# Optimization experiments

Measured on AMD Instinct MI355X. Metric: run time of the kernel, lower is better.

## Reference

```python
import jax, jax.numpy as jnp
import numpy as np

B, QL, KL, D, H = 2, 512, 8192, 1024, 8
HD = D // H  # head dim = 128


def setup_inputs() -> dict:
    key = jax.random.key(0)
    ks = jax.random.split(key, 12)
    s = 0.02
    return {
        "inputs_q": jax.random.normal(ks[0], (B, QL, D), jnp.float32),
        "inputs_k": jax.random.normal(ks[1], (B, KL, D), jnp.float32),
        "inputs_v": jax.random.normal(ks[2], (B, KL, D), jnp.float32),
        "attention_mask": jax.random.randint(ks[3], (B, QL, KL), 0, 2).astype(bool),
        "Wq": jax.random.normal(ks[4], (D, D), jnp.float32) * s,
        "bq": jnp.zeros((D,), jnp.float32),
        "Wk": jax.random.normal(ks[5], (D, D), jnp.float32) * s,
        "bk": jnp.zeros((D,), jnp.float32),
        "Wv": jax.random.normal(ks[6], (D, D), jnp.float32) * s,
        "bv": jnp.zeros((D,), jnp.float32),
        "Wf": jax.random.normal(ks[7], (D, D), jnp.float32) * s,
        "bf": jnp.zeros((D,), jnp.float32),
    }


def reference(inputs_q, inputs_k, inputs_v, attention_mask, Wq, bq, Wk, bk, Wv, bv, Wf, bf):
    # Projections (torch Linear: x @ W.T + b)
    q = inputs_q @ Wq.T + bq  # [B, QL, D]
    k = inputs_k @ Wk.T + bk  # [B, KL, D]
    v = inputs_v @ Wv.T + bv  # [B, KL, D]

    q = q.reshape(B, QL, H, HD)
    k = k.reshape(B, KL, H, HD)
    v = v.reshape(B, KL, H, HD)

    # scores [B, H, QL, KL]
    scores = jnp.einsum("bqhd,bkhd->bhqk", q, k)
    scale = 1.0 / np.sqrt(HD).astype(np.float32)
    scores = scores * scale
    large_k = jnp.float32(1e30)
    scores = jnp.where(attention_mask[:, None, :, :], scores, -large_k)

    probs = jax.nn.softmax(scores, axis=-1)
    # note: original calls self.dropout(normalized) but discards the result -> no-op

    summed = jnp.einsum("bhqk,bkhd->bqhd", probs, v).reshape(B, QL, H * HD)

    # wipe rows whose mask is all zero
    wipe = jnp.all(~attention_mask, axis=2, keepdims=True)  # [B, QL, 1]
    summed = jnp.where(wipe, jnp.zeros_like(summed), summed)

    return summed @ Wf.T + bf
```

## Files before the change

### kernel.cpp

```cpp
#include <hip/hip_runtime.h>
#include <hip/hip_bf16.h>
#include <math.h>

typedef __attribute__((ext_vector_type(4))) float fx4;
typedef __attribute__((ext_vector_type(4))) short sx4;
typedef __attribute__((ext_vector_type(8))) short sx8;
typedef unsigned long long u64;

#define MFMA16(a, b, c) __builtin_amdgcn_mfma_f32_16x16x16bf16_1k(a, b, c, 0, 0, 0)
#define MFMA32(a, b, c) __builtin_amdgcn_mfma_f32_16x16x32_bf16(a, b, c, 0, 0, 0)

__device__ __forceinline__ unsigned short f2bf(float f) {
  unsigned int u = __float_as_uint(f);
  return (unsigned short)((u + 0x7fffu + ((u >> 16) & 1u)) >> 16);
}

__device__ __forceinline__ unsigned cvtpk(float lo, float hi) {
  unsigned r;
  asm("v_cvt_pk_bf16_f32 %0, %1, %2" : "=v"(r) : "v"(lo), "v"(hi));
  return r;
}

typedef const __attribute__((address_space(1))) char* gc1p;
typedef __attribute__((address_space(3))) char* lc3p;
__device__ __forceinline__ void glds16(const void* g, const void* lds_uniform) {
  gc1p gp = (gc1p)(unsigned long long)(uintptr_t)g;
  lc3p lp = (lc3p)(unsigned)__builtin_amdgcn_readfirstlane((int)(unsigned)(uintptr_t)lds_uniform);
  __builtin_amdgcn_global_load_lds(gp, lp, 16, 0, 0);
}

__global__ __launch_bounds__(256) void k_prep(
    const float* __restrict__ Wq, const float* __restrict__ Wk,
    const float* __restrict__ Wv, const float* __restrict__ Wf, short* cwq,
    short* cwk, short* cwv, short* cwf) {
  const int bx = blockIdx.x;
  const int t = threadIdx.x;
  const int seg = bx >> 6;
  const float* s = seg == 0 ? Wq : seg == 1 ? Wk : seg == 2 ? Wv : Wf;
  short* d = seg == 0 ? cwq : seg == 1 ? cwk : seg == 2 ? cwv : cwf;
  const size_t base = (size_t)(bx & 63) * 16384;
#pragma unroll
  for (int it = 0; it < 4; it++) {
    const size_t i = base + (size_t)it * 4096 + (size_t)t * 16;
    const fx4 a0 = *(const fx4*)(s + i);
    const fx4 a1 = *(const fx4*)(s + i + 4);
    const fx4 a2 = *(const fx4*)(s + i + 8);
    const fx4 a3 = *(const fx4*)(s + i + 12);
    sx8 o0, o1;
    o0[0] = (short)f2bf(a0[0]); o0[1] = (short)f2bf(a0[1]);
    o0[2] = (short)f2bf(a0[2]); o0[3] = (short)f2bf(a0[3]);
    o0[4] = (short)f2bf(a1[0]); o0[5] = (short)f2bf(a1[1]);
    o0[6] = (short)f2bf(a1[2]); o0[7] = (short)f2bf(a1[3]);
    o1[0] = (short)f2bf(a2[0]); o1[1] = (short)f2bf(a2[1]);
    o1[2] = (short)f2bf(a2[2]); o1[3] = (short)f2bf(a2[3]);
    o1[4] = (short)f2bf(a3[0]); o1[5] = (short)f2bf(a3[1]);
    o1[6] = (short)f2bf(a3[2]); o1[7] = (short)f2bf(a3[3]);
    *(sx8*)(d + i) = o0;
    *(sx8*)(d + i + 8) = o1;
  }
}

template <int MODE, int MT>
__device__ __forceinline__ void gemm_pipe(short* sA, short* sB,
                                          const float* __restrict__ Af,
                                          const short* __restrict__ Bw,
                                          const float* __restrict__ bias,
                                          void* __restrict__ Cptr, int M, int N,
                                          float alpha, int bx) {
  constexpr int K = 1024;
  constexpr int NT = 16;
  const int tid = threadIdx.x;
  const int lane = tid & 63;
  const int w = tid >> 6;
  const int quad = lane >> 4;
  const int l16 = lane & 15;
  const int x7 = l16 & 7;
  int m0, n0;
  if (M >= 8192) {
    const int ml = bx & 7, nn = (bx >> 3) & 7, mh = bx >> 6;
    m0 = (mh * 8 + ml) * MT;
    n0 = nn << 7;
  } else {
    const int ntile = N >> 7;
    n0 = (bx % ntile) << 7;
    m0 = (bx / ntile) * MT;
  }
  constexpr int NI = (MT == 128) ? 4 : 2;
  constexpr int NJ = (MT == 128) ? 4 : 2;
  const int wm = (MT == 128) ? ((w >> 1) << 6) : 0;
  const int wn = (MT == 128) ? ((w & 1) << 6) : (w << 5);
  const fx4 fzero = {0.f, 0.f, 0.f, 0.f};
  fx4 acc[4][NI];
#pragma unroll
  for (int i = 0; i < 4; i++)
#pragma unroll
    for (int j = 0; j < NI; j++) acc[i][j] = fzero;

  const int srow = lane >> 3;
  const int scb = lane & 7;
  fx4 ra[2][NJ][2];

  auto ISSUE_B = [&](int t) {
#pragma unroll
    for (int j = 0; j < 4; j++) {
      const int row = w * 32 + j * 8 + srow;
      const int cb = scb ^ (row & 7);
      glds16(Bw + (size_t)(n0 + row) * K + t * 64 + cb * 8,
             &sB[(t & 1) * 8192 + (w * 32 + j * 8) * 64]);
    }
  };
  auto ISSUE_A = [&](int t, int slot) {
#pragma unroll
    for (int j = 0; j < NJ; j++) {
      const int rbase = (MT == 128) ? (w * 32 + j * 8) : (j * 32 + w * 8);
      const int row = rbase + srow;
      const int cb = scb ^ (row & 7);
      const float* src = Af + (size_t)(m0 + row) * K + t * 64 + cb * 8;
      ra[slot][j][0] = *(const fx4*)src;
      ra[slot][j][1] = *(const fx4*)(src + 4);
    }
  };
  auto CVT_A = [&](int t, int slot) {
#pragma unroll
    for (int j = 0; j < NJ; j++) {
      const int rbase = (MT == 128) ? (w * 32 + j * 8) : (j * 32 + w * 8);
      sx8 o;
      unsigned* ou = (unsigned*)&o;
      ou[0] = cvtpk(ra[slot][j][0][0], ra[slot][j][0][1]);
      ou[1] = cvtpk(ra[slot][j][0][2], ra[slot][j][0][3]);
      ou[2] = cvtpk(ra[slot][j][1][0], ra[slot][j][1][1]);
      ou[3] = cvtpk(ra[slot][j][1][2], ra[slot][j][1][3]);
      *(sx8*)(&sA[(t & 1) * 8192 + rbase * 64 + lane * 8]) = o;
    }
  };
  auto COMPUTE = [&](int t) {
    const short* pA = sA + (t & 1) * 8192;
    const short* pB = sB + (t & 1) * 8192;
#pragma unroll
    for (int kc = 0; kc < 2; kc++) {
      const int cbp = ((kc * 4 + quad) ^ x7) * 8;
      sx8 fa[4], fb[NI];
#pragma unroll
      for (int i = 0; i < 4; i++)
        fa[i] = *(const sx8*)(&pA[(wm + i * 16 + l16) * 64 + cbp]);
#pragma unroll
      for (int i = 0; i < NI; i++)
        fb[i] = *(const sx8*)(&pB[(wn + i * 16 + l16) * 64 + cbp]);
#pragma unroll
      for (int mi = 0; mi < 4; mi++)
#pragma unroll
        for (int ni = 0; ni < NI; ni++)
          acc[mi][ni] = MFMA32(fa[mi], fb[ni], acc[mi][ni]);
    }
  };

  ISSUE_B(0);
  __builtin_amdgcn_sched_barrier(0);
  ISSUE_A(0, 0);
  __builtin_amdgcn_sched_barrier(0);
  ISSUE_B(1);
  __builtin_amdgcn_sched_barrier(0);
  ISSUE_A(1, 1);
  __builtin_amdgcn_sched_barrier(0);
  CVT_A(0, 0);
  asm volatile("s_waitcnt lgkmcnt(0)\n\ts_barrier" ::: "memory");

#pragma unroll
  for (int t = 0; t < NT; ++t) {
    if (t + 1 < NT) ISSUE_B(t + 1);
    __builtin_amdgcn_sched_barrier(0);
    if (t + 2 < NT) ISSUE_A(t + 2, t & 1);
    __builtin_amdgcn_sched_barrier(0);
    COMPUTE(t);
    if (t + 1 < NT) CVT_A(t + 1, (t + 1) & 1);
    if (t + 2 < NT) {
      if (MT == 128)
        asm volatile("s_waitcnt vmcnt(8) lgkmcnt(0)\n\ts_barrier" ::: "memory");
      else
        asm volatile("s_waitcnt vmcnt(4) lgkmcnt(0)\n\ts_barrier" ::: "memory");
    } else if (t + 1 < NT) {
      asm volatile("s_waitcnt vmcnt(0) lgkmcnt(0)\n\ts_barrier" ::: "memory");
    }
  }
#pragma unroll
  for (int ni = 0; ni < NI; ni++) {
    const int col = n0 + wn + ni * 16 + l16;
    const float bval = bias[col];
    if (MODE == 2) {
#pragma unroll
      for (int mi = 0; mi < 4; mi++) {
        const int rowb = m0 + wm + mi * 16 + quad * 4;
        const int bb = rowb >> 13;
        const int kl = (rowb & 8191) ^ ((col & 8) ? 4 : 0);
        sx4 pkv;
#pragma unroll
        for (int r = 0; r < 4; r++) pkv[r] = (short)f2bf(acc[mi][ni][r] + bval);
        *(sx4*)((unsigned short*)Cptr + ((size_t)bb * 1024 + col) * 8192 + kl) = pkv;
      }
    } else {
#pragma unroll
      for (int mi = 0; mi < 4; mi++)
#pragma unroll
        for (int r = 0; r < 4; r++) {
          const int row = m0 + wm + mi * 16 + quad * 4 + r;
          const float v = (acc[mi][ni][r] + bval) * alpha;
          ((unsigned short*)Cptr)[(size_t)row * N + col] = f2bf(v);
        }
    }
  }
}

__device__ __forceinline__ void gemm_out_body(short* sA, short* sB,
                                              const short* __restrict__ A,
                                              const short* __restrict__ Bw,
                                              const float* __restrict__ bias,
                                              float* __restrict__ Cptr, int N,
                                              int K, int bx) {
  constexpr int MT = 64;
  const int tid = threadIdx.x;
  const int lane = tid & 63;
  const int w = tid >> 6;
  const int quad = lane >> 4;
  const int l16 = lane & 15;
  const int x7 = l16 & 7;
  const int ntile = N >> 7;
  const int n0 = (bx % ntile) << 7;
  const int m0 = (bx / ntile) * MT;
  constexpr int NI = 2;
  const int wm = 0;
  const int wn = w << 5;
  const fx4 fzero = {0.f, 0.f, 0.f, 0.f};
  fx4 acc[4][NI];
#pragma unroll
  for (int i = 0; i < 4; i++)
#pragma unroll
    for (int j = 0; j < NI; j++) acc[i][j] = fzero;
  const int srow = lane >> 3;
  const int scb = lane & 7;

#pragma unroll
  for (int j = 0; j < 2; j++) {
    const int rbase = j * 32 + w * 8;
    const int row = rbase + srow;
    const int cb = scb ^ (row & 7);
    glds16(A + (size_t)(m0 + row) * K + cb * 8, &sA[rbase * 64]);
  }
#pragma unroll
  for (int j = 0; j < 4; j++) {
    const int row = w * 32 + j * 8 + srow;
    const int cb = scb ^ (row & 7);
    glds16(Bw + (size_t)(n0 + row) * K + cb * 8, &sB[(w * 32 + j * 8) * 64]);
  }
  __syncthreads();

  int buf = 0;
  for (int k0 = 0; k0 < K; k0 += 64) {
    const int nb = buf ^ 1;
    if (k0 + 64 < K) {
#pragma unroll
      for (int j = 0; j < 4; j++) {
        const int row = w * 32 + j * 8 + srow;
        const int cb = scb ^ (row & 7);
        glds16(Bw + (size_t)(n0 + row) * K + (k0 + 64) + cb * 8,
               &sB[nb * 8192 + (w * 32 + j * 8) * 64]);
      }
#pragma unroll
      for (int j = 0; j < 2; j++) {
        const int rbase = j * 32 + w * 8;
        const int row = rbase + srow;
        const int cb = scb ^ (row & 7);
        glds16(A + (size_t)(m0 + row) * K + (k0 + 64) + cb * 8,
               &sA[nb * 8192 + rbase * 64]);
      }
    }
    const short* pA = sA + buf * 8192;
    const short* pB = sB + buf * 8192;
#pragma unroll
    for (int kc = 0; kc < 2; kc++) {
      const int cbp = ((kc * 4 + quad) ^ x7) * 8;
      sx8 fa[4], fb[NI];
#pragma unroll
      for (int i = 0; i < 4; i++)
        fa[i] = *(const sx8*)(&pA[(wm + i * 16 + l16) * 64 + cbp]);
#pragma unroll
      for (int i = 0; i < NI; i++)
        fb[i] = *(const sx8*)(&pB[(wn + i * 16 + l16) * 64 + cbp]);
#pragma unroll
      for (int mi = 0; mi < 4; mi++)
#pragma unroll
        for (int ni = 0; ni < NI; ni++)
          acc[mi][ni] = MFMA32(fa[mi], fb[ni], acc[mi][ni]);
    }
    __syncthreads();
    buf = nb;
  }
#pragma unroll
  for (int ni = 0; ni < NI; ni++) {
    const int col = n0 + wn + ni * 16 + l16;
    const float bval = bias[col];
#pragma unroll
    for (int mi = 0; mi < 4; mi++)
#pragma unroll
      for (int r = 0; r < 4; r++) {
        const int row = m0 + wm + mi * 16 + quad * 4 + r;
        Cptr[(size_t)row * N + col] = acc[mi][ni][r] + bval;
      }
  }
}

__global__ __launch_bounds__(256, 2) void k_proj(
    const float* __restrict__ ink, const short* __restrict__ cwk,
    const float* __restrict__ bk, short* __restrict__ Kp,
    const float* __restrict__ inv, const short* __restrict__ cwv,
    const float* __restrict__ bv, short* __restrict__ Vt,
    const float* __restrict__ inq, const short* __restrict__ cwq,
    const float* __restrict__ bq, short* __restrict__ Qp, float alpha_q,
    const int* __restrict__ mask, u64* __restrict__ mb) {
  __shared__ __align__(16) short smem[32768];
  const int bx = blockIdx.x;
  if (bx >= 2176) {
    unsigned char(*nib)[256] = (unsigned char(*)[256])smem;
    const int t = threadIdx.x;
    const int mrow0 = (bx - 2176) * 4;
#pragma unroll
    for (int j = 0; j < 4; j++) {
      const int4 m = *(const int4*)(mask + (size_t)(mrow0 + j) * 1024 + t * 4);
      nib[j][t] = (unsigned char)((m.x != 0) | ((m.y != 0) << 1) |
                                  ((m.z != 0) << 2) | ((m.w != 0) << 3));
    }
    __syncthreads();
    if (t < 64) {
      const int j = t >> 4, i = t & 15;
      u64 wv = 0;
#pragma unroll
      for (int k = 0; k < 16; k++)
        wv |= (u64)(nib[j][i * 16 + k] & 0xF) << (4 * k);
      mb[(size_t)(mrow0 + j) * 16 + i] = wv;
    }
    return;
  }
  if (bx < 1024)
    gemm_pipe<0, 128>(smem, smem + 16384, ink, cwk, bk, Kp, 16384, 1024, 1.f,
                      bx);
  else if (bx < 2048)
    gemm_pipe<2, 128>(smem, smem + 16384, inv, cwv, bv, Vt, 16384, 1024, 1.f,
                      bx - 1024);
  else
    gemm_pipe<0, 64>(smem, smem + 16384, inq, cwq, bq, Qp, 1024, 1024, alpha_q,
                     bx - 2048);
}

__global__ __launch_bounds__(256) void k_gemm_out(const short* __restrict__ summed,
                                                  const short* __restrict__ cwf,
                                                  const float* __restrict__ bf,
                                                  float* __restrict__ out) {
  __shared__ __align__(16) short smem[32768];
  gemm_out_body(smem, smem + 16384, summed, cwf, bf, out, 1024, 1024,
                blockIdx.x);
}

__global__ __launch_bounds__(256, 4) void k_attn(const short* __restrict__ Qp,
                                                 const short* __restrict__ Kp,
                                                 const short* __restrict__ Vt,
                                                 const u64* __restrict__ mb,
                                                 float* __restrict__ ml,
                                                 float* __restrict__ Op) {
  __shared__ __align__(16) short sK[8192];
  __shared__ __align__(16) short sV[8192];
  const int x = blockIdx.x;
  const int gl = x & 7;
  const int qt = (x >> 3) & 7;
  const int gh = x >> 6;
  const int g = gh * 8 + gl;
  const int s = g & 7;
  const int h = (g >> 3) & 7;
  const int b = g >> 6;
  const int li = ((b * 8 + h) * 8 + qt) * 8 + s;
  const int t = threadIdx.x;
  const int lane = t & 63;
  const int w = t >> 6;
  const int quad = lane >> 4;
  const int l16 = lane & 15;
  const int x7 = l16 & 7;
  const int q0 = qt << 6;
  const fx4 fzero = {0.f, 0.f, 0.f, 0.f};

  const short* qbase = Qp + (size_t)(b * 512 + q0 + w * 16 + l16) * 1024 + h * 128;
  sx8 aq[4];
#pragma unroll
  for (int kc = 0; kc < 4; kc++) aq[kc] = *(const sx8*)(qbase + kc * 32 + quad * 8);

  fx4 Ot[8];
#pragma unroll
  for (int d = 0; d < 8; d++) Ot[d] = fzero;
  float lsum = 0.f;

  const short* kbase = Kp + (size_t)(b * 8192 + s * 1024) * 1024 + h * 128;
  const short* vbase = Vt + (size_t)(b * 1024 + h * 128) * 8192 + s * 1024;
  const u64* wdp = mb + (size_t)(b * 512 + q0 + w * 16 + l16) * 128 + s * 16;
  const int srow4 = lane >> 4, scb16 = lane & 15;
  const int srow8 = lane >> 3, scb8 = lane & 7;
  const int h4 = ((quad & 1) ^ ((l16 >> 3) & 1)) * 4;

  for (int kt = 0; kt < 16; kt++) {
    __syncthreads();
#pragma unroll
    for (int j = 0; j < 4; j++) {
      const int row = (w * 4 + j) * 4 + srow4;
      const int cb = scb16 ^ (row & 7);
      glds16(kbase + (size_t)(kt * 64 + row) * 1024 + cb * 8, &sK[(w * 4 + j) * 512]);
    }
#pragma unroll
    for (int j = 0; j < 4; j++) {
      const int row = (w * 4 + j) * 8 + srow8;
      const int cb = scb8 ^ (row & 7);
      glds16(vbase + (size_t)row * 8192 + kt * 64 + cb * 8, &sV[(w * 4 + j) * 512]);
    }
    const u64 wd = wdp[kt];
    __syncthreads();
    const unsigned lo = (unsigned)wd, hi = (unsigned)(wd >> 32);
    sx4 pk[4];
#pragma unroll
    for (int nt = 0; nt < 4; nt++) {
      fx4 a = fzero;
      __builtin_amdgcn_s_setprio(1);
#pragma unroll
      for (int kc = 0; kc < 4; kc++) {
        const sx8 kf = *(const sx8*)(&sK[(nt * 16 + l16) * 128 + ((kc * 4 + quad) ^ x7) * 8]);
        a = MFMA32(kf, aq[kc], a);
      }
      __builtin_amdgcn_s_setprio(0);
      const unsigned bits = (nt & 2) ? hi : lo;
      const int sh = (nt & 1) * 16 + quad * 4;
      float pv[4];
#pragma unroll
      for (int r = 0; r < 4; r++) {
        const float e = __builtin_amdgcn_exp2f(a[r]);
        pv[r] = ((bits >> (sh + r)) & 1u) ? e : 0.f;
        lsum += pv[r];
      }
      sx4 pko;
      ((unsigned*)&pko)[0] = __builtin_amdgcn_perm(
          __float_as_uint(pv[1]) + 0x8000u, __float_as_uint(pv[0]) + 0x8000u, 0x07060302u);
      ((unsigned*)&pko)[1] = __builtin_amdgcn_perm(
          __float_as_uint(pv[3]) + 0x8000u, __float_as_uint(pv[2]) + 0x8000u, 0x07060302u);
      pk[nt] = pko;
    }
    __builtin_amdgcn_s_setprio(1);
#pragma unroll
    for (int dt = 0; dt < 8; dt++) {
      fx4 o = Ot[dt];
#pragma unroll
      for (int nt = 0; nt < 4; nt++) {
        const int cb = (2 * nt + (quad >> 1)) ^ x7;
        const sx4 vf = *(const sx4*)(&sV[(dt * 16 + l16) * 64 + cb * 8 + h4]);
        o = MFMA16(vf, pk[nt], o);
      }
      Ot[dt] = o;
    }
    __builtin_amdgcn_s_setprio(0);
  }
  lsum += __shfl_xor(lsum, 16, 64);
  lsum += __shfl_xor(lsum, 32, 64);
  if (lane < 16) ml[(size_t)li * 64 + w * 16 + l16] = lsum;
  float* ob = Op + (size_t)li * 8192 + (w * 16 + l16) * 128 + quad * 4;
#pragma unroll
  for (int dt = 0; dt < 8; dt++) *(fx4*)(ob + dt * 16) = Ot[dt];
}

__global__ __launch_bounds__(256) void k_combine(const float* __restrict__ ml,
                                                 const float* __restrict__ Op,
                                                 short* __restrict__ summed) {
  const int bx = blockIdx.x;
  const int xc = bx >> 1;
  const int dh = (bx & 1) * 64;
  const int qt = xc & 7;
  const int h = (xc >> 3) & 7;
  const int b = xc >> 6;
  const int t = threadIdx.x;
  const int row = t >> 2;
  const int dg = dh + (t & 3) * 16;
  float L = 0.f;
#pragma unroll
  for (int s = 0; s < 8; s++) L += ml[(size_t)(xc * 8 + s) * 64 + row];
  float o[16];
#pragma unroll
  for (int i = 0; i < 16; i++) o[i] = 0.f;
  if (L != 0.f) {
#pragma unroll
    for (int s = 0; s < 8; s++) {
      const float* src = Op + (size_t)(xc * 8 + s) * 8192 + row * 128 + dg;
#pragma unroll
      for (int i = 0; i < 4; i++) {
        const fx4 v = *(const fx4*)(src + i * 4);
        o[i * 4 + 0] += v[0]; o[i * 4 + 1] += v[1];
        o[i * 4 + 2] += v[2]; o[i * 4 + 3] += v[3];
      }
    }
    const float inv = 1.f / L;
#pragma unroll
    for (int i = 0; i < 16; i++) o[i] *= inv;
  }
  short* dst = summed + (size_t)(b * 512 + qt * 64 + row) * 1024 + h * 128 + dg;
#pragma unroll
  for (int i = 0; i < 2; i++) {
    sx8 pkv;
#pragma unroll
    for (int j = 0; j < 8; j++) pkv[j] = (short)f2bf(o[i * 8 + j]);
    *(sx8*)(dst + i * 8) = pkv;
  }
}

extern "C" void kernel_launch(void* const* d_in, const int* in_sizes, int n_in,
                              void* d_out, int out_size, void* d_ws, size_t ws_size,
                              hipStream_t stream) {
  (void)in_sizes; (void)n_in; (void)out_size; (void)ws_size;
  const float* inq = (const float*)d_in[0];
  const float* ink = (const float*)d_in[1];
  const float* inv = (const float*)d_in[2];
  const int* mask = (const int*)d_in[3];
  const float* Wq = (const float*)d_in[4];
  const float* bq = (const float*)d_in[5];
  const float* Wk = (const float*)d_in[6];
  const float* bk = (const float*)d_in[7];
  const float* Wv = (const float*)d_in[8];
  const float* bv = (const float*)d_in[9];
  const float* Wf = (const float*)d_in[10];
  const float* bf = (const float*)d_in[11];

  char* ws = (char*)d_ws;
  short* Vt = (short*)(ws + 0);
  short* Kp = (short*)(ws + 33554432);
  float* Op = (float*)(ws + 67108864);
  short* cwq = (short*)(ws + 102760448);
  short* cwk = (short*)(ws + 104857600);
  short* cwv = (short*)(ws + 106954752);
  short* cwf = (short*)(ws + 109051904);
  short* Qp = (short*)(ws + 111149056);
  short* summed = (short*)(ws + 113246208);
  u64* mb = (u64*)(ws + 115343360);
  float* ml = (float*)(ws + 116391936);

  const float alpha_q = 0.12751757f;

  k_prep<<<256, 256, 0, stream>>>(Wq, Wk, Wv, Wf, cwq, cwk, cwv, cwf);
  k_proj<<<4224, 256, 0, stream>>>(ink, cwk, bk, Kp, inv, cwv, bv, Vt, inq, cwq,
                                   bq, Qp, alpha_q, mask, mb);
  k_attn<<<1024, 256, 0, stream>>>(Qp, Kp, Vt, mb, ml, Op);
  k_combine<<<256, 256, 0, stream>>>(ml, Op, summed);
  k_gemm_out<<<128, 256, 0, stream>>>(summed, cwf, bf, (float*)d_out);
}
```

Baseline: 351.5 us.

## Double-buffer K/V tiles in attention kernel to overlap loads with MFMA

The attention kernel now allocates two LDS buffers each for K and V. It prefetches tile kt+1 while computing on tile kt, with a single waitcnt+barrier at the end of each iteration in place of two syncthreads. The goal is to hide global-to-LDS load latency behind the QK and PV MFMA work. In exchange, LDS use doubles and launch bounds drop from 4 to 2 blocks per SM, which lowers occupancy and the latency hiding that came from running several blocks at once.

```diff
diff --git a/kernel.cpp b/kernel.cpp
--- a/kernel.cpp
+++ b/kernel.cpp
@@ -359,14 +359,14 @@
                 blockIdx.x);
 }
 
-__global__ __launch_bounds__(256, 4) void k_attn(const short* __restrict__ Qp,
+__global__ __launch_bounds__(256, 2) void k_attn(const short* __restrict__ Qp,
                                                  const short* __restrict__ Kp,
                                                  const short* __restrict__ Vt,
                                                  const u64* __restrict__ mb,
                                                  float* __restrict__ ml,
                                                  float* __restrict__ Op) {
-  __shared__ __align__(16) short sK[8192];
-  __shared__ __align__(16) short sV[8192];
+  __shared__ __align__(16) short sK[16384];
+  __shared__ __align__(16) short sV[16384];
   const int x = blockIdx.x;
   const int gl = x & 7;
   const int qt = (x >> 3) & 7;
@@ -402,22 +402,40 @@
   const int srow8 = lane >> 3, scb8 = lane & 7;
   const int h4 = ((quad & 1) ^ ((l16 >> 3) & 1)) * 4;
 
+#pragma unroll
+  for (int j = 0; j < 4; j++) {
+    const int row = (w * 4 + j) * 4 + srow4;
+    const int cb = scb16 ^ (row & 7);
+    glds16(kbase + (size_t)row * 1024 + cb * 8, &sK[(w * 4 + j) * 512]);
+  }
+#pragma unroll
+  for (int j = 0; j < 4; j++) {
+    const int row = (w * 4 + j) * 8 + srow8;
+    const int cb = scb8 ^ (row & 7);
+    glds16(vbase + (size_t)row * 8192 + cb * 8, &sV[(w * 4 + j) * 512]);
+  }
+  asm volatile("s_waitcnt vmcnt(0) lgkmcnt(0)\n\ts_barrier" ::: "memory");
+
   for (int kt = 0; kt < 16; kt++) {
-    __syncthreads();
-#pragma unroll
-    for (int j = 0; j < 4; j++) {
-      const int row = (w * 4 + j) * 4 + srow4;
-      const int cb = scb16 ^ (row & 7);
-      glds16(kbase + (size_t)(kt * 64 + row) * 1024 + cb * 8, &sK[(w * 4 + j) * 512]);
-    }
-#pragma unroll
-    for (int j = 0; j < 4; j++) {
-      const int row = (w * 4 + j) * 8 + srow8;
-      const int cb = scb8 ^ (row & 7);
-      glds16(vbase + (size_t)row * 8192 + kt * 64 + cb * 8, &sV[(w * 4 + j) * 512]);
+    const int cur = (kt & 1) * 8192;
+    const int nxt = 8192 - cur;
+    if (kt < 15) {
+#pragma unroll
+      for (int j = 0; j < 4; j++) {
+        const int row = (w * 4 + j) * 4 + srow4;
+        const int cb = scb16 ^ (row & 7);
+        glds16(kbase + (size_t)((kt + 1) * 64 + row) * 1024 + cb * 8,
+               &sK[nxt + (w * 4 + j) * 512]);
+      }
+#pragma unroll
+      for (int j = 0; j < 4; j++) {
+        const int row = (w * 4 + j) * 8 + srow8;
+        const int cb = scb8 ^ (row & 7);
+        glds16(vbase + (size_t)row * 8192 + (kt + 1) * 64 + cb * 8,
+               &sV[nxt + (w * 4 + j) * 512]);
+      }
     }
     const u64 wd = wdp[kt];
-    __syncthreads();
     const unsigned lo = (unsigned)wd, hi = (unsigned)(wd >> 32);
     sx4 pk[4];
 #pragma unroll
@@ -426,7 +444,8 @@
       __builtin_amdgcn_s_setprio(1);
 #pragma unroll
       for (int kc = 0; kc < 4; kc++) {
-        const sx8 kf = *(const sx8*)(&sK[(nt * 16 + l16) * 128 + ((kc * 4 + quad) ^ x7) * 8]);
+        const sx8 kf = *(const sx8*)(&sK[cur + (nt * 16 + l16) * 128 +
+                                         ((kc * 4 + quad) ^ x7) * 8]);
         a = MFMA32(kf, aq[kc], a);
       }
       __builtin_amdgcn_s_setprio(0);
@@ -453,12 +472,13 @@
 #pragma unroll
       for (int nt = 0; nt < 4; nt++) {
         const int cb = (2 * nt + (quad >> 1)) ^ x7;
-        const sx4 vf = *(const sx4*)(&sV[(dt * 16 + l16) * 64 + cb * 8 + h4]);
+        const sx4 vf = *(const sx4*)(&sV[cur + (dt * 16 + l16) * 64 + cb * 8 + h4]);
         o = MFMA16(vf, pk[nt], o);
       }
       Ot[dt] = o;
     }
     __builtin_amdgcn_s_setprio(0);
+    asm volatile("s_waitcnt vmcnt(0) lgkmcnt(0)\n\ts_barrier" ::: "memory");
   }
   lsum += __shfl_xor(lsum, 16, 64);
   lsum += __shfl_xor(lsum, 32, 64);
```

New measurement: 364.9 us. 1.04x slower.

## Enlarge projection GEMM tiles to 256x256 with 512-thread blocks

Applied to the files above, without the earlier changes.

Replaces the 128x128 (and 64x128) projection GEMM tiles with 256x256 tiles computed by 8 waves, each owning a 128x64 sub-tile with a 32-accumulator MFMA block. The larger tiles halve global reads per output element for the fp32 activations and bf16 weights. The pipeline is also simplified from a two-stage register prefetch with sched barriers to a single-stage prefetch with two barriers per K step. In exchange, each block uses 128KB of LDS, so only one block can be resident per CU even though launch bounds request two. Register use also rises sharply, and less latency hiding may leave the MFMA units idle.

```diff
diff --git a/kernel.cpp b/kernel.cpp
--- a/kernel.cpp
+++ b/kernel.cpp
@@ -60,15 +60,11 @@
   }
 }
 
-template <int MODE, int MT>
-__device__ __forceinline__ void gemm_pipe(short* sA, short* sB,
-                                          const float* __restrict__ Af,
-                                          const short* __restrict__ Bw,
-                                          const float* __restrict__ bias,
-                                          void* __restrict__ Cptr, int M, int N,
-                                          float alpha, int bx) {
+__device__ __forceinline__ void gemm256_body(
+    short* sA, short* sB, const float* __restrict__ Af,
+    const short* __restrict__ Bw, const float* __restrict__ bias,
+    void* __restrict__ Cptr, int M, float alpha, int mode, int bx) {
   constexpr int K = 1024;
-  constexpr int NT = 16;
   const int tid = threadIdx.x;
   const int lane = tid & 63;
   const int w = tid >> 6;
@@ -77,118 +73,101 @@
   const int x7 = l16 & 7;
   int m0, n0;
   if (M >= 8192) {
-    const int ml = bx & 7, nn = (bx >> 3) & 7, mh = bx >> 6;
-    m0 = (mh * 8 + ml) * MT;
-    n0 = nn << 7;
+    const int xcd = bx & 7, idx = bx >> 3;
+    m0 = ((idx >> 2) * 8 + xcd) << 8;
+    n0 = (idx & 3) << 8;
   } else {
-    const int ntile = N >> 7;
-    n0 = (bx % ntile) << 7;
-    m0 = (bx / ntile) * MT;
-  }
-  constexpr int NI = (MT == 128) ? 4 : 2;
-  constexpr int NJ = (MT == 128) ? 4 : 2;
-  const int wm = (MT == 128) ? ((w >> 1) << 6) : 0;
-  const int wn = (MT == 128) ? ((w & 1) << 6) : (w << 5);
+    m0 = (bx >> 2) << 8;
+    n0 = (bx & 3) << 8;
+  }
+  const int wm = (w >> 2) << 7;
+  const int wn = (w & 3) << 6;
   const fx4 fzero = {0.f, 0.f, 0.f, 0.f};
-  fx4 acc[4][NI];
-#pragma unroll
-  for (int i = 0; i < 4; i++)
-#pragma unroll
-    for (int j = 0; j < NI; j++) acc[i][j] = fzero;
-
-  const int srow = lane >> 3;
-  const int scb = lane & 7;
-  fx4 ra[2][NJ][2];
-
-  auto ISSUE_B = [&](int t) {
+  fx4 acc[8][4];
+#pragma unroll
+  for (int i = 0; i < 8; i++)
+#pragma unroll
+    for (int j = 0; j < 4; j++) acc[i][j] = fzero;
+
+  const int arow = tid >> 3;
+  const int acb = tid & 7;
+  const int brow = w * 8 + (lane >> 3);
+  const int bcb = lane & 7;
+  fx4 ra[4][2];
+
+#pragma unroll
+  for (int j = 0; j < 4; j++) {
+    const int row = j * 64 + brow;
+    const int cb = bcb ^ (row & 7);
+    glds16(Bw + (size_t)(n0 + row) * K + cb * 8, &sB[(j * 64 + w * 8) * 64]);
+  }
+#pragma unroll
+  for (int j = 0; j < 4; j++) {
+    const int row = j * 64 + arow;
+    const int cb = acb ^ (row & 7);
+    const float* src = Af + (size_t)(m0 + row) * K + cb * 8;
+    ra[j][0] = *(const fx4*)src;
+    ra[j][1] = *(const fx4*)(src + 4);
+  }
+
+  for (int t = 0; t < 16; ++t) {
+    const int boff = (t & 1) << 14;
+    const int nboff = boff ^ 16384;
 #pragma unroll
     for (int j = 0; j < 4; j++) {
-      const int row = w * 32 + j * 8 + srow;
-      const int cb = scb ^ (row & 7);
-      glds16(Bw + (size_t)(n0 + row) * K + t * 64 + cb * 8,
-             &sB[(t & 1) * 8192 + (w * 32 + j * 8) * 64]);
-    }
-  };
-  auto ISSUE_A = [&](int t, int slot) {
-#pragma unroll
-    for (int j = 0; j < NJ; j++) {
-      const int rbase = (MT == 128) ? (w * 32 + j * 8) : (j * 32 + w * 8);
-      const int row = rbase + srow;
-      const int cb = scb ^ (row & 7);
-      const float* src = Af + (size_t)(m0 + row) * K + t * 64 + cb * 8;
-      ra[slot][j][0] = *(const fx4*)src;
-      ra[slot][j][1] = *(const fx4*)(src + 4);
-    }
-  };
-  auto CVT_A = [&](int t, int slot) {
-#pragma unroll
-    for (int j = 0; j < NJ; j++) {
-      const int rbase = (MT == 128) ? (w * 32 + j * 8) : (j * 32 + w * 8);
       sx8 o;
       unsigned* ou = (unsigned*)&o;
-      ou[0] = cvtpk(ra[slot][j][0][0], ra[slot][j][0][1]);
-      ou[1] = cvtpk(ra[slot][j][0][2], ra[slot][j][0][3]);
-      ou[2] = cvtpk(ra[slot][j][1][0], ra[slot][j][1][1]);
-      ou[3] = cvtpk(ra[slot][j][1][2], ra[slot][j][1][3]);
-      *(sx8*)(&sA[(t & 1) * 8192 + rbase * 64 + lane * 8]) = o;
-    }
-  };
-  auto COMPUTE = [&](int t) {
-    const short* pA = sA + (t & 1) * 8192;
-    const short* pB = sB + (t & 1) * 8192;
+      ou[0] = cvtpk(ra[j][0][0], ra[j][0][1]);
+      ou[1] = cvtpk(ra[j][0][2], ra[j][0][3]);
+      ou[2] = cvtpk(ra[j][1][0], ra[j][1][1]);
+      ou[3] = cvtpk(ra[j][1][2], ra[j][1][3]);
+      *(sx8*)(&sA[boff + j * 4096 + tid * 8]) = o;
+    }
+    if (t < 15) {
+#pragma unroll
+      for (int j = 0; j < 4; j++) {
+        const int row = j * 64 + brow;
+        const int cb = bcb ^ (row & 7);
+        glds16(Bw + (size_t)(n0 + row) * K + (t + 1) * 64 + cb * 8,
+               &sB[nboff + (j * 64 + w * 8) * 64]);
+      }
+#pragma unroll
+      for (int j = 0; j < 4; j++) {
+        const int row = j * 64 + arow;
+        const int cb = acb ^ (row & 7);
+        const float* src = Af + (size_t)(m0 + row) * K + (t + 1) * 64 + cb * 8;
+        ra[j][0] = *(const fx4*)src;
+        ra[j][1] = *(const fx4*)(src + 4);
+      }
+    }
+    asm volatile("s_waitcnt lgkmcnt(0)\n\ts_barrier" ::: "memory");
+    const short* pA = sA + boff;
+    const short* pB = sB + boff;
 #pragma unroll
     for (int kc = 0; kc < 2; kc++) {
       const int cbp = ((kc * 4 + quad) ^ x7) * 8;
-      sx8 fa[4], fb[NI];
+      sx8 fa[8], fb[4];
+#pragma unroll
+      for (int i = 0; i < 8; i++)
+        fa[i] = *(const sx8*)(&pA[(wm + i * 16 + l16) * 64 + cbp]);
 #pragma unroll
       for (int i = 0; i < 4; i++)
-        fa[i] = *(const sx8*)(&pA[(wm + i * 16 + l16) * 64 + cbp]);
-#pragma unroll
-      for (int i = 0; i < NI; i++)
         fb[i] = *(const sx8*)(&pB[(wn + i * 16 + l16) * 64 + cbp]);
 #pragma unroll
-      for (int mi = 0; mi < 4; mi++)
-#pragma unroll
-        for (int ni = 0; ni < NI; ni++)
+      for (int mi = 0; mi < 8; mi++)
+#pragma unroll
+        for (int ni = 0; ni < 4; ni++)
           acc[mi][ni] = MFMA32(fa[mi], fb[ni], acc[mi][ni]);
     }
-  };
-
-  ISSUE_B(0);
-  __builtin_amdgcn_sched_barrier(0);
-  ISSUE_A(0, 0);
-  __builtin_amdgcn_sched_barrier(0);
-  ISSUE_B(1);
-  __builtin_amdgcn_sched_barrier(0);
-  ISSUE_A(1, 1);
-  __builtin_amdgcn_sched_barrier(0);
-  CVT_A(0, 0);
-  asm volatile("s_waitcnt lgkmcnt(0)\n\ts_barrier" ::: "memory");
-
-#pragma unroll
-  for (int t = 0; t < NT; ++t) {
-    if (t + 1 < NT) ISSUE_B(t + 1);
-    __builtin_amdgcn_sched_barrier(0);
-    if (t + 2 < NT) ISSUE_A(t + 2, t & 1);
-    __builtin_amdgcn_sched_barrier(0);
-    COMPUTE(t);
-    if (t + 1 < NT) CVT_A(t + 1, (t + 1) & 1);
-    if (t + 2 < NT) {
-      if (MT == 128)
-        asm volatile("s_waitcnt vmcnt(8) lgkmcnt(0)\n\ts_barrier" ::: "memory");
-      else
-        asm volatile("s_waitcnt vmcnt(4) lgkmcnt(0)\n\ts_barrier" ::: "memory");
-    } else if (t + 1 < NT) {
-      asm volatile("s_waitcnt vmcnt(0) lgkmcnt(0)\n\ts_barrier" ::: "memory");
-    }
-  }
-#pragma unroll
-  for (int ni = 0; ni < NI; ni++) {
+    asm volatile("s_waitcnt lgkmcnt(0)\n\ts_barrier" ::: "memory");
+  }
+#pragma unroll
+  for (int ni = 0; ni < 4; ni++) {
     const int col = n0 + wn + ni * 16 + l16;
     const float bval = bias[col];
-    if (MODE == 2) {
-#pragma unroll
-      for (int mi = 0; mi < 4; mi++) {
+    if (mode == 2) {
+#pragma unroll
+      for (int mi = 0; mi < 8; mi++) {
         const int rowb = m0 + wm + mi * 16 + quad * 4;
         const int bb = rowb >> 13;
         const int kl = (rowb & 8191) ^ ((col & 8) ? 4 : 0);
@@ -199,15 +178,57 @@
       }
     } else {
 #pragma unroll
-      for (int mi = 0; mi < 4; mi++)
+      for (int mi = 0; mi < 8; mi++)
 #pragma unroll
         for (int r = 0; r < 4; r++) {
           const int row = m0 + wm + mi * 16 + quad * 4 + r;
           const float v = (acc[mi][ni][r] + bval) * alpha;
-          ((unsigned short*)Cptr)[(size_t)row * N + col] = f2bf(v);
+          ((unsigned short*)Cptr)[(size_t)row * 1024 + col] = f2bf(v);
         }
     }
   }
+}
+
+__global__ __launch_bounds__(512, 2) void k_proj(
+    const float* __restrict__ ink, const short* __restrict__ cwk,
+    const float* __restrict__ bk, short* __restrict__ Kp,
+    const float* __restrict__ inv, const short* __restrict__ cwv,
+    const float* __restrict__ bv, short* __restrict__ Vt,
+    const float* __restrict__ inq, const short* __restrict__ cwq,
+    const float* __restrict__ bq, short* __restrict__ Qp, float alpha_q,
+    const int* __restrict__ mask, u64* __restrict__ mb) {
+  __shared__ __align__(16) short smem[65536];
+  const int bx = blockIdx.x;
+  if (bx >= 528) {
+    unsigned char(*nib)[256] = (unsigned char(*)[256])smem;
+    const int t = threadIdx.x;
+    const int mrow0 = (bx - 528) * 4;
+    if (t < 256) {
+#pragma unroll
+      for (int j = 0; j < 4; j++) {
+        const int4 m = *(const int4*)(mask + (size_t)(mrow0 + j) * 1024 + t * 4);
+        nib[j][t] = (unsigned char)((m.x != 0) | ((m.y != 0) << 1) |
+                                    ((m.z != 0) << 2) | ((m.w != 0) << 3));
+      }
+    }
+    __syncthreads();
+    if (t < 64) {
+      const int j = t >> 4, i = t & 15;
+      u64 wv = 0;
+#pragma unroll
+      for (int k = 0; k < 16; k++)
+        wv |= (u64)(nib[j][i * 16 + k] & 0xF) << (4 * k);
+      mb[(size_t)(mrow0 + j) * 16 + i] = wv;
+    }
+    return;
+  }
+  if (bx < 256)
+    gemm256_body(smem, smem + 32768, ink, cwk, bk, Kp, 16384, 1.f, 0, bx);
+  else if (bx < 512)
+    gemm256_body(smem, smem + 32768, inv, cwv, bv, Vt, 16384, 1.f, 2, bx - 256);
+  else
+    gemm256_body(smem, smem + 32768, inq, cwq, bq, Qp, 1024, alpha_q, 0,
+                 bx - 512);
 }
 
 __device__ __forceinline__ void gemm_out_body(short* sA, short* sB,
@@ -306,48 +327,6 @@
         Cptr[(size_t)row * N + col] = acc[mi][ni][r] + bval;
       }
   }
-}
-
-__global__ __launch_bounds__(256, 2) void k_proj(
-    const float* __restrict__ ink, const short* __restrict__ cwk,
-    const float* __restrict__ bk, short* __restrict__ Kp,
-    const float* __restrict__ inv, const short* __restrict__ cwv,
-    const float* __restrict__ bv, short* __restrict__ Vt,
-    const float* __restrict__ inq, const short* __restrict__ cwq,
-    const float* __restrict__ bq, short* __restrict__ Qp, float alpha_q,
-    const int* __restrict__ mask, u64* __restrict__ mb) {
-  __shared__ __align__(16) short smem[32768];
-  const int bx = blockIdx.x;
-  if (bx >= 2176) {
-    unsigned char(*nib)[256] = (unsigned char(*)[256])smem;
-    const int t = threadIdx.x;
-    const int mrow0 = (bx - 2176) * 4;
-#pragma unroll
-    for (int j = 0; j < 4; j++) {
-      const int4 m = *(const int4*)(mask + (size_t)(mrow0 + j) * 1024 + t * 4);
-      nib[j][t] = (unsigned char)((m.x != 0) | ((m.y != 0) << 1) |
-                                  ((m.z != 0) << 2) | ((m.w != 0) << 3));
-    }
-    __syncthreads();
-    if (t < 64) {
-      const int j = t >> 4, i = t & 15;
-      u64 wv = 0;
-#pragma unroll
-      for (int k = 0; k < 16; k++)
-        wv |= (u64)(nib[j][i * 16 + k] & 0xF) << (4 * k);
-      mb[(size_t)(mrow0 + j) * 16 + i] = wv;
-    }
-    return;
-  }
-  if (bx < 1024)
-    gemm_pipe<0, 128>(smem, smem + 16384, ink, cwk, bk, Kp, 16384, 1024, 1.f,
-                      bx);
-  else if (bx < 2048)
-    gemm_pipe<2, 128>(smem, smem + 16384, inv, cwv, bv, Vt, 16384, 1024, 1.f,
-                      bx - 1024);
-  else
-    gemm_pipe<0, 64>(smem, smem + 16384, inq, cwq, bq, Qp, 1024, 1024, alpha_q,
-                     bx - 2048);
 }
 
 __global__ __launch_bounds__(256) void k_gemm_out(const short* __restrict__ summed,
@@ -544,7 +523,7 @@
   const float alpha_q = 0.12751757f;
 
   k_prep<<<256, 256, 0, stream>>>(Wq, Wk, Wv, Wf, cwq, cwk, cwv, cwf);
-  k_proj<<<4224, 256, 0, stream>>>(ink, cwk, bk, Kp, inv, cwv, bv, Vt, inq, cwq,
+  k_proj<<<2576, 512, 0, stream>>>(ink, cwk, bk, Kp, inv, cwv, bv, Vt, inq, cwq,
                                    bq, Qp, alpha_q, mask, mb);
   k_attn<<<1024, 256, 0, stream>>>(Qp, Kp, Vt, mb, ml, Op);
   k_combine<<<256, 256, 0, stream>>>(ml, Op, summed);
```

Result: slower. 377.5 us (+7.4%).
